# Performance work log

Measured on AMD Instinct MI355X. Metric: run time of the kernel, lower is better.

## Reference

```python
import jax, jax.numpy as jnp
import numpy as np

B = 8192
N_COLS = 64
D = 1024
EPS = 1e-5


def _layernorm(x, g, b):
    m = jnp.mean(x, axis=-1, keepdims=True)
    v = jnp.mean(jnp.square(x - m), axis=-1, keepdims=True)
    return (x - m) * jax.lax.rsqrt(v + EPS) * g + b


def setup_inputs() -> dict:
    key = jax.random.key(0)
    ks = jax.random.split(key, 8)
    s = 0.02
    return {
        "x1_enc": jax.random.normal(ks[0], (1, N_COLS, D), jnp.float32),
        "x2_enc": jax.random.normal(ks[1], (B, D), jnp.float32),
        "We": jax.random.normal(ks[2], (4, 2 * D, D), jnp.float32) * s,
        "be": jnp.zeros((4, D), jnp.float32),
        "W1": jax.random.normal(ks[3], (2 * D, 4 * D), jnp.float32) * s,
        "b1": jnp.zeros((4 * D,), jnp.float32),
        "g1": jnp.ones((4 * D,), jnp.float32),
        "bt1": jnp.zeros((4 * D,), jnp.float32),
        "W2": jax.random.normal(ks[4], (4 * D, 2 * D), jnp.float32) * s,
        "b2": jnp.zeros((2 * D,), jnp.float32),
        "g2": jnp.ones((2 * D,), jnp.float32),
        "bt2": jnp.zeros((2 * D,), jnp.float32),
        "W3": jax.random.normal(ks[5], (2 * D, 1), jnp.float32) * s,
        "b3": jnp.zeros((1,), jnp.float32),
        "col_pairs": jax.random.randint(ks[6], (B, 2), 0, N_COLS, jnp.int64),
        "vis_type": jax.random.randint(ks[7], (B,), 0, 4, jnp.int64),
    }


def reference(x1_enc, x2_enc, We, be, W1, b1, g1, bt1, W2, b2, g2, bt2, W3, b3,
              col_pairs, vis_type):
    # x1 repeated B times is identical per row -> gather directly from x1_enc[0]
    x11 = x1_enc[0, col_pairs[:, 0]]          # [B, D]
    x12 = x1_enc[0, col_pairs[:, 1]]          # [B, D]
    x1c = jnp.concatenate([x11, x12], axis=1)  # [B, 2D]

    # 1-of-4 expert routing: compute all experts, select by vis_type
    all_y = jax.nn.relu(jnp.einsum('bd,edk->bek', x1c, We) + be)  # [B, 4, D]
    y1 = jnp.take_along_axis(all_y, vis_type[:, None, None], axis=1)[:, 0]  # [B, D]

    y = jnp.concatenate([y1, x2_enc], axis=1)  # [B, 2D]
    h = _layernorm(jax.nn.relu(y @ W1 + b1), g1, bt1)
    h = _layernorm(jax.nn.relu(h @ W2 + b2), g2, bt2)
    return jax.nn.sigmoid(h @ W3 + b3)  # [B, 1]
```

## Files before the change

kernel.cpp:

```cpp
#include <hip/hip_runtime.h>

typedef unsigned short u16;
typedef __bf16 bf16x8 __attribute__((ext_vector_type(8)));
typedef float f32x4v __attribute__((ext_vector_type(4)));
typedef u16 u16x8 __attribute__((ext_vector_type(8)));

__device__ __forceinline__ u16 f2bf(float f) {
  union { float f; unsigned u; } v; v.f = f;
  unsigned r = v.u + 0x7fffu + ((v.u >> 16) & 1u);
  return (u16)(r >> 16);
}
__device__ __forceinline__ float bf2f(u16 h) {
  union { unsigned u; float f; } v; v.u = ((unsigned)h) << 16;
  return v.f;
}

#define G2L16(g, l)                                                            \
  __builtin_amdgcn_global_load_lds((__attribute__((address_space(1))) void*)(g), \
                                   (__attribute__((address_space(3))) void*)(l), 16, 0, 0)

__global__ __launch_bounds__(256) void k_transpose2(const float* __restrict__ W1,
                                                    u16* __restrict__ W1T,
                                                    const float* __restrict__ W2,
                                                    u16* __restrict__ W2gT,
                                                    const float* __restrict__ g1,
                                                    const float* __restrict__ bt1,
                                                    float* __restrict__ w2ps,
                                                    float* __restrict__ w2pc) {
  __shared__ float tile[64][65];
  int bid = blockIdx.x;
  const float* in;
  u16* out;
  int R, C, bx, by, fold;
  if (bid < 2048) {
    in = W1; out = W1T; R = 2048; C = 4096; fold = 0;
    bx = bid & 63; by = bid >> 6;
  } else {
    bid -= 2048;
    in = W2; out = W2gT; R = 4096; C = 2048; fold = 1;
    bx = bid & 31; by = bid >> 5;
  }
  const int c0 = bx * 64, r0 = by * 64;
  const int t = threadIdx.x;
  const int tc = (t & 15) * 4, tr = t >> 4;
#pragma unroll
  for (int i = 0; i < 4; ++i) {
    int r = tr + i * 16;
    f32x4v v = *(const f32x4v*)(in + (size_t)(r0 + r) * C + c0 + tc);
    tile[r][tc] = v[0]; tile[r][tc + 1] = v[1];
    tile[r][tc + 2] = v[2]; tile[r][tc + 3] = v[3];
  }
  __syncthreads();
  const int oc = t >> 2;
  const int rb = (t & 3) * 16;
  float gv[16];
#pragma unroll
  for (int i = 0; i < 16; ++i) gv[i] = fold ? g1[r0 + rb + i] : 1.f;
  u16x8 o0, o1;
#pragma unroll
  for (int i = 0; i < 8; ++i) o0[i] = f2bf(tile[rb + i][oc] * gv[i]);
#pragma unroll
  for (int i = 0; i < 8; ++i) o1[i] = f2bf(tile[rb + 8 + i][oc] * gv[8 + i]);
  *(u16x8*)(out + (size_t)(c0 + oc) * R + r0 + rb) = o0;
  *(u16x8*)(out + (size_t)(c0 + oc) * R + r0 + rb + 8) = o1;
  if (fold) {
    float ps = 0.f, pc = 0.f;
#pragma unroll
    for (int i = 0; i < 16; ++i) {
      float w = tile[rb + i][oc];
      ps += gv[i] * w;
      pc += bt1[r0 + rb + i] * w;
    }
    ps += __shfl_down(ps, 2, 4); ps += __shfl_down(ps, 1, 4);
    pc += __shfl_down(pc, 2, 4); pc += __shfl_down(pc, 1, 4);
    if ((t & 3) == 0) {
      w2ps[(size_t)by * 2048 + c0 + oc] = ps;
      w2pc[(size_t)by * 2048 + c0 + oc] = pc;
    }
  }
}

__global__ __launch_bounds__(256) void k_pq(const float* __restrict__ x1,
                                            const float* __restrict__ We,
                                            float* __restrict__ pq) {
  const int n0 = blockIdx.x * 64;
  const int ep = blockIdx.y;
  const int e = ep >> 1, p = ep & 1;
  const int chalf = blockIdx.z;
  __shared__ float As[32][33];
  __shared__ float Bs[32][68];
  const int t = threadIdx.x;
  const int tx = t & 15, ty = t >> 4;
  float acc[2][4] = {};
  const float* wbase = We + (size_t)e * 2048 * 1024 + (size_t)p * 1024 * 1024;
  for (int k0 = 0; k0 < 1024; k0 += 32) {
#pragma unroll
    for (int i = 0; i < 4; ++i) {
      int ix = t + i * 256;
      As[ix >> 5][ix & 31] =
          x1[(size_t)(chalf * 32 + (ix >> 5)) * 1024 + k0 + (ix & 31)];
    }
#pragma unroll
    for (int i = 0; i < 8; ++i) {
      int ix = t + i * 256;
      Bs[ix >> 6][ix & 63] = wbase[(size_t)(k0 + (ix >> 6)) * 1024 + n0 + (ix & 63)];
    }
    __syncthreads();
#pragma unroll
    for (int kk = 0; kk < 32; ++kk) {
      float av[2];
#pragma unroll
      for (int i = 0; i < 2; ++i) av[i] = As[ty * 2 + i][kk];
      f32x4v bv = *(const f32x4v*)&Bs[kk][tx * 4];
#pragma unroll
      for (int i = 0; i < 2; ++i)
#pragma unroll
        for (int j = 0; j < 4; ++j) acc[i][j] += av[i] * bv[j];
    }
    __syncthreads();
  }
#pragma unroll
  for (int i = 0; i < 2; ++i) {
    float* dst = pq + ((size_t)ep * 64 + chalf * 32 + ty * 2 + i) * 1024 + n0 + tx * 4;
#pragma unroll
    for (int j = 0; j < 4; ++j) dst[j] = acc[i][j];
  }
}

__global__ __launch_bounds__(256) void k_build_y(const float* __restrict__ pq,
                                                 const float* __restrict__ x2,
                                                 const float* __restrict__ be,
                                                 const int* __restrict__ cp,
                                                 const int* __restrict__ vis,
                                                 u16* __restrict__ Y) {
  const int t = threadIdx.x;
  for (int rr = 0; rr < 8; ++rr) {
    const int b = blockIdx.x * 8 + rr;
    const int e = vis[b];
    u16x8 o;
    if (t < 128) {
      const int c0 = cp[2 * b], c1 = cp[2 * b + 1];
      const size_t po = ((size_t)(e * 2) * 64 + c0) * 1024 + t * 8;
      const size_t qo = ((size_t)(e * 2 + 1) * 64 + c1) * 1024 + t * 8;
      const float* B = be + e * 1024 + t * 8;
#pragma unroll
      for (int i = 0; i < 8; ++i) {
        float v = pq[po + i] + pq[qo + i] + B[i];
        o[i] = f2bf(v > 0.f ? v : 0.f);
      }
      *(u16x8*)(Y + (size_t)b * 2048 + t * 8) = o;
    } else {
      const float* X = x2 + (size_t)b * 1024 + (size_t)(t - 128) * 8;
#pragma unroll
      for (int i = 0; i < 8; ++i) o[i] = f2bf(X[i]);
      *(u16x8*)(Y + (size_t)b * 2048 + 1024 + (size_t)(t - 128) * 8) = o;
    }
  }
}

#define BARRIER __builtin_amdgcn_s_barrier()
#define WLG0                                                    \
  do {                                                          \
    asm volatile("s_waitcnt lgkmcnt(0)" ::: "memory");          \
    __builtin_amdgcn_sched_barrier(0);                          \
  } while (0)
#define WVM(n) asm volatile("s_waitcnt vmcnt(" #n ")" ::: "memory")

template <int MODE>
__global__ __launch_bounds__(512, 2) void k_gemm(const u16* __restrict__ A,
                                                 const u16* __restrict__ BT,
                                                 const float* __restrict__ bias,
                                                 const float2* __restrict__ stats,
                                                 const float* __restrict__ s1,
                                                 const float* __restrict__ c1b,
                                                 const float* __restrict__ gw3,
                                                 float2* __restrict__ sp_out,
                                                 float4* __restrict__ part,
                                                 u16* __restrict__ C,
                                                 int M, int N, int K) {
  __shared__ u16 smem[65536];
  const int tid = threadIdx.x;
  const int lane = tid & 63;
  const int wave = tid >> 6;
  const int wm = wave >> 2;
  const int wn = wave & 3;

  const int nx = gridDim.x, ny = gridDim.y;
  const int bid = blockIdx.y * nx + blockIdx.x;
  const int stripe = ny >> 3;
  const int xcd = bid & 7;
  const int loc = bid >> 3;
  const int by = xcd * stripe + (loc % stripe);
  const int bx = loc / stripe;
  const int tileM = by * 256;
  const int tileN = bx * 256;

  f32x4v acc[8][4];
#pragma unroll
  for (int i = 0; i < 8; ++i)
#pragma unroll
    for (int j = 0; j < 4; ++j) acc[i][j] = (f32x4v){0.f, 0.f, 0.f, 0.f};

  const int srow = tid >> 3;
  const int slc = ((tid & 7) ^ (srow & 7)) * 8;
  const u16* aG = A + (size_t)(tileM + srow) * K + slc;
  const u16* bG = BT + (size_t)(tileN + srow) * K + slc;

#define STAGE(ab, h, buf, kt)                                                  \
  do {                                                                         \
    u16* dst_ = smem + (buf) * 32768 + (ab) * 16384 + (h) * 8192 + tid * 8;    \
    const u16* g_ = ((ab) ? bG : aG) + (size_t)(h) * 128 * K + (size_t)(kt) * 64; \
    G2L16(g_, dst_);                                                           \
    G2L16(g_ + (size_t)64 * K, dst_ + 4096);                                   \
  } while (0)

  const int kp0 = (((lane >> 4) ^ (lane & 7)) * 8);
  const int kp1 = kp0 ^ 32;
  const int awoff = wm * 8192 + (lane & 15) * 64;
  const int bwoff = (wn >> 1) * 8192 + ((wn & 1) * 64 + (lane & 15)) * 64;

  bf16x8 af[2][4], bfr[2][4];

#define RD_A(buf, mh)                                                          \
  do {                                                                         \
    const u16* ap_ = smem + (buf) * 32768 + awoff;                             \
    _Pragma("unroll") for (int q = 0; q < 4; ++q) {                            \
      af[0][q] = *(const bf16x8*)(ap_ + ((mh) * 4 + q) * 1024 + kp0);          \
      af[1][q] = *(const bf16x8*)(ap_ + ((mh) * 4 + q) * 1024 + kp1);          \
    }                                                                          \
  } while (0)

#define RD_B(buf, nh)                                                          \
  do {                                                                         \
    const u16* bp_ = smem + (buf) * 32768 + 16384 + bwoff;                     \
    _Pragma("unroll") for (int q = 0; q < 2; ++q) {                            \
      bfr[0][(nh) * 2 + q] = *(const bf16x8*)(bp_ + ((nh) * 2 + q) * 1024 + kp0); \
      bfr[1][(nh) * 2 + q] = *(const bf16x8*)(bp_ + ((nh) * 2 + q) * 1024 + kp1); \
    }                                                                          \
  } while (0)

#define QUAD(mh, nh)                                                           \
  do {                                                                         \
    __builtin_amdgcn_s_setprio(1);                                             \
    _Pragma("unroll") for (int kh = 0; kh < 2; ++kh)                           \
    _Pragma("unroll") for (int q = 0; q < 4; ++q)                              \
    _Pragma("unroll") for (int p = 0; p < 2; ++p)                              \
      acc[(mh) * 4 + q][(nh) * 2 + p] = __builtin_amdgcn_mfma_f32_16x16x32_bf16( \
          af[kh][q], bfr[kh][(nh) * 2 + p], acc[(mh) * 4 + q][(nh) * 2 + p], 0, 0, 0); \
    __builtin_amdgcn_s_setprio(0);                                             \
  } while (0)

  const int nkt = K >> 6;
  const int niter = nkt >> 1;

  STAGE(1, 0, 0, 0);
  STAGE(1, 1, 0, 0);
  STAGE(0, 0, 0, 0);
  STAGE(0, 1, 0, 0);
  STAGE(1, 0, 1, 1);
  STAGE(1, 1, 1, 1);
  STAGE(0, 0, 1, 1);
  WVM(6);
  BARRIER;

  for (int it = 0; it < niter; ++it) {
    const int t1 = 2 * it + 1;
    int t2 = 2 * it + 2; if (t2 >= nkt) t2 = nkt - 1;
    int t3 = 2 * it + 3; if (t3 >= nkt) t3 = nkt - 1;
    RD_A(0, 0); RD_B(0, 0);
    STAGE(0, 1, 1, t1);
    BARRIER; WLG0; QUAD(0, 0); BARRIER;
    RD_B(0, 1);
    BARRIER; WLG0; QUAD(0, 1); BARRIER;
    RD_A(0, 1);
    STAGE(1, 0, 0, t2);
    BARRIER; WLG0; QUAD(1, 0); BARRIER;
    STAGE(1, 1, 0, t2);
    STAGE(0, 0, 0, t2);
    BARRIER; QUAD(1, 1); WVM(6); BARRIER;
    RD_A(1, 0); RD_B(1, 0);
    STAGE(0, 1, 0, t2);
    BARRIER; WLG0; QUAD(0, 0); BARRIER;
    RD_B(1, 1);
    BARRIER; WLG0; QUAD(0, 1); BARRIER;
    RD_A(1, 1);
    STAGE(1, 0, 1, t3);
    BARRIER; WLG0; QUAD(1, 0); BARRIER;
    STAGE(1, 1, 1, t3);
    STAGE(0, 0, 1, t3);
    BARRIER; QUAD(1, 1); WVM(6); BARRIER;
  }

  const int crow = tileM + wm * 128 + (lane >> 4) * 4;
  const int ccol = tileN + wn * 64 + (lane & 15);
  float cv0[4], cv1[4], cg[4];
#pragma unroll
  for (int ni = 0; ni < 4; ++ni) {
    const int c = ccol + ni * 16;
    if (MODE == 0) {
      cv0[ni] = bias[c];
    } else {
      cv0[ni] = s1[c];
      cv1[ni] = c1b[c];
      cg[ni] = gw3[c];
    }
  }
  const int cb = bx * 4 + wn;
#pragma unroll
  for (int mi = 0; mi < 8; ++mi) {
#pragma unroll
    for (int r = 0; r < 4; ++r) {
      const int row = crow + mi * 16 + r;
      if (MODE == 0) {
        float s_ = 0.f, ss_ = 0.f;
#pragma unroll
        for (int ni = 0; ni < 4; ++ni) {
          float v = acc[mi][ni][r] + cv0[ni];
          v = v > 0.f ? v : 0.f;
          s_ += v; ss_ += v * v;
          C[(size_t)row * N + ccol + ni * 16] = f2bf(v);
        }
#pragma unroll
        for (int off = 8; off >= 1; off >>= 1) {
          s_ += __shfl_xor(s_, off, 16);
          ss_ += __shfl_xor(ss_, off, 16);
        }
        if ((lane & 15) == 0)
          sp_out[(size_t)row * 64 + cb] = make_float2(s_, ss_);
      } else {
        float2 st = stats[row];
        const float m = st.x, rs = st.y;
        float s_ = 0.f, ss_ = 0.f, d_ = 0.f;
#pragma unroll
        for (int ni = 0; ni < 4; ++ni) {
          float v = rs * acc[mi][ni][r] - rs * m * cv0[ni] + cv1[ni];
          v = v > 0.f ? v : 0.f;
          s_ += v; ss_ += v * v; d_ += v * cg[ni];
        }
#pragma unroll
        for (int off = 8; off >= 1; off >>= 1) {
          s_ += __shfl_xor(s_, off, 16);
          ss_ += __shfl_xor(ss_, off, 16);
          d_ += __shfl_xor(d_, off, 16);
        }
        if ((lane & 15) == 0)
          part[(size_t)row * 32 + cb] = make_float4(s_, ss_, d_, 0.f);
      }
    }
  }
}

__global__ __launch_bounds__(256) void k_reduce(const float2* __restrict__ sp,
                                                float2* __restrict__ stats,
                                                const float* __restrict__ w2ps,
                                                const float* __restrict__ w2pc,
                                                const float* __restrict__ b2,
                                                float* __restrict__ s1,
                                                float* __restrict__ c1b,
                                                const float* __restrict__ g2,
                                                const float* __restrict__ bt2,
                                                const float* __restrict__ W3,
                                                float* __restrict__ gw3,
                                                float* __restrict__ scal) {
  __shared__ float red[8];
  const int bid = blockIdx.x;
  const int t = threadIdx.x;
  if (bid < 32) {
    const int g = t >> 4, l = t & 15;
#pragma unroll 1
    for (int rr = 0; rr < 16; ++rr) {
      const int row = bid * 256 + rr * 16 + g;
      float s = 0.f, ss = 0.f;
#pragma unroll
      for (int i = 0; i < 4; ++i) {
        float2 p = sp[(size_t)row * 64 + l * 4 + i];
        s += p.x; ss += p.y;
      }
#pragma unroll
      for (int off = 8; off >= 1; off >>= 1) {
        s += __shfl_xor(s, off, 16);
        ss += __shfl_xor(ss, off, 16);
      }
      if (l == 0) {
        float m = s * (1.f / 4096.f);
        float var = ss * (1.f / 4096.f) - m * m;
        stats[row] = make_float2(m, rsqrtf(var + 1e-5f));
      }
    }
  } else if (bid < 40) {
    const int nn = (bid - 32) * 256 + t;
    float s = 0.f, c = 0.f;
    for (int kb = 0; kb < 64; ++kb) {
      s += w2ps[(size_t)kb * 2048 + nn];
      c += w2pc[(size_t)kb * 2048 + nn];
    }
    s1[nn] = s;
    c1b[nn] = c + b2[nn];
  } else {
    float sg = 0.f, cb = 0.f;
    for (int i = 0; i < 8; ++i) {
      int c = i * 256 + t;
      float w3 = W3[c];
      float gv = g2[c] * w3;
      gw3[c] = gv;
      sg += gv;
      cb += bt2[c] * w3;
    }
#pragma unroll
    for (int off = 32; off > 0; off >>= 1) {
      sg += __shfl_down(sg, off, 64);
      cb += __shfl_down(cb, off, 64);
    }
    const int lane = t & 63, wv = t >> 6;
    if (lane == 0) { red[wv] = sg; red[4 + wv] = cb; }
    __syncthreads();
    if (t == 0) {
      scal[0] = red[0] + red[1] + red[2] + red[3];
      scal[1] = red[4] + red[5] + red[6] + red[7];
    }
  }
}

__global__ __launch_bounds__(256) void k_final(const float4* __restrict__ part,
                                               const float* __restrict__ scal,
                                               const float* __restrict__ b3,
                                               float* __restrict__ out) {
  const int t = threadIdx.x;
  const int g = t >> 4, l = t & 15;
  const int row = blockIdx.x * 16 + g;
  float4 a = part[(size_t)row * 32 + l * 2];
  float4 b = part[(size_t)row * 32 + l * 2 + 1];
  float S = a.x + b.x, SS = a.y + b.y, D = a.z + b.z;
#pragma unroll
  for (int off = 8; off >= 1; off >>= 1) {
    S += __shfl_xor(S, off, 16);
    SS += __shfl_xor(SS, off, 16);
    D += __shfl_xor(D, off, 16);
  }
  if (l == 0) {
    float m = S * (1.f / 2048.f);
    float rs = rsqrtf(SS * (1.f / 2048.f) - m * m + 1e-5f);
    float logit = rs * D - rs * m * scal[0] + scal[1] + b3[0];
    out[row] = 1.f / (1.f + expf(-logit));
  }
}

extern "C" void kernel_launch(void* const* d_in, const int* in_sizes, int n_in,
                              void* d_out, int out_size, void* d_ws, size_t ws_size,
                              hipStream_t stream) {
  const float* x1 = (const float*)d_in[0];
  const float* x2 = (const float*)d_in[1];
  const float* We = (const float*)d_in[2];
  const float* be = (const float*)d_in[3];
  const float* W1 = (const float*)d_in[4];
  const float* b1 = (const float*)d_in[5];
  const float* g1 = (const float*)d_in[6];
  const float* bt1 = (const float*)d_in[7];
  const float* W2 = (const float*)d_in[8];
  const float* b2 = (const float*)d_in[9];
  const float* g2 = (const float*)d_in[10];
  const float* bt2 = (const float*)d_in[11];
  const float* W3 = (const float*)d_in[12];
  const float* b3 = (const float*)d_in[13];
  const int* cp = (const int*)d_in[14];
  const int* vis = (const int*)d_in[15];
  float* out = (float*)d_out;

  char* ws = (char*)d_ws;
  u16* W1T  = (u16*)(ws);
  u16* W2gT = (u16*)(ws + 16777216);
  u16* Y    = (u16*)(ws + 33554432);
  u16* H1   = (u16*)(ws + 67108864);
  float* PQ = (float*)(ws + 134217728);
  float2* sp = (float2*)(ws + 134217728);
  float4* part = (float4*)(ws + 134217728);
  float2* stats = (float2*)(ws + 138412032);
  float* s1   = (float*)(ws + 138477568);
  float* c1b  = (float*)(ws + 138485760);
  float* w2ps = (float*)(ws + 138493952);
  float* w2pc = (float*)(ws + 139018240);
  float* gw3  = (float*)(ws + 139542528);
  float* scal = (float*)(ws + 139550720);

  k_transpose2<<<4096, 256, 0, stream>>>(W1, W1T, W2, W2gT, g1, bt1, w2ps, w2pc);
  k_pq<<<dim3(16, 8, 2), 256, 0, stream>>>(x1, We, PQ);
  k_build_y<<<1024, 256, 0, stream>>>(PQ, x2, be, cp, vis, Y);
  k_gemm<0><<<dim3(16, 32), 512, 0, stream>>>(
      Y, W1T, b1, nullptr, nullptr, nullptr, nullptr, sp, nullptr, H1,
      8192, 4096, 2048);
  k_reduce<<<41, 256, 0, stream>>>(sp, stats, w2ps, w2pc, b2, s1, c1b,
                                   g2, bt2, W3, gw3, scal);
  k_gemm<1><<<dim3(8, 32), 512, 0, stream>>>(
      H1, W2gT, nullptr, stats, s1, c1b, gw3, nullptr, part, nullptr,
      8192, 2048, 4096);
  k_final<<<512, 256, 0, stream>>>(part, scal, b3, out);
}
```

Before: 468.9 us.

## Merge weight prep kernels and rework GEMM LDS read/stage pipeline schedule

```diff
diff --git a/kernel.cpp b/kernel.cpp
--- a/kernel.cpp
+++ b/kernel.cpp
@@ -19,111 +19,113 @@
   __builtin_amdgcn_global_load_lds((__attribute__((address_space(1))) void*)(g), \
                                    (__attribute__((address_space(3))) void*)(l), 16, 0, 0)
 
-__global__ __launch_bounds__(256) void k_transpose2(const float* __restrict__ W1,
-                                                    u16* __restrict__ W1T,
-                                                    const float* __restrict__ W2,
-                                                    u16* __restrict__ W2gT,
-                                                    const float* __restrict__ g1,
-                                                    const float* __restrict__ bt1,
-                                                    float* __restrict__ w2ps,
-                                                    float* __restrict__ w2pc) {
-  __shared__ float tile[64][65];
+__global__ __launch_bounds__(256) void k_prep(const float* __restrict__ W1,
+                                              u16* __restrict__ W1T,
+                                              const float* __restrict__ W2,
+                                              u16* __restrict__ W2gT,
+                                              const float* __restrict__ g1,
+                                              const float* __restrict__ bt1,
+                                              float* __restrict__ w2ps,
+                                              float* __restrict__ w2pc,
+                                              const float* __restrict__ x1,
+                                              const float* __restrict__ We,
+                                              float* __restrict__ pq) {
+  __shared__ float lds[4224];
   int bid = blockIdx.x;
-  const float* in;
-  u16* out;
-  int R, C, bx, by, fold;
-  if (bid < 2048) {
-    in = W1; out = W1T; R = 2048; C = 4096; fold = 0;
-    bx = bid & 63; by = bid >> 6;
+  const int t = threadIdx.x;
+  if (bid < 4096) {
+    float (*tile)[65] = (float(*)[65])lds;
+    const float* in;
+    u16* out;
+    int R, C, bx, by, fold;
+    if (bid < 2048) {
+      in = W1; out = W1T; R = 2048; C = 4096; fold = 0;
+      bx = bid & 63; by = bid >> 6;
+    } else {
+      bid -= 2048;
+      in = W2; out = W2gT; R = 4096; C = 2048; fold = 1;
+      bx = bid & 31; by = bid >> 5;
+    }
+    const int c0 = bx * 64, r0 = by * 64;
+    const int tc = (t & 15) * 4, tr = t >> 4;
+#pragma unroll
+    for (int i = 0; i < 4; ++i) {
+      int r = tr + i * 16;
+      f32x4v v = *(const f32x4v*)(in + (size_t)(r0 + r) * C + c0 + tc);
+      tile[r][tc] = v[0]; tile[r][tc + 1] = v[1];
+      tile[r][tc + 2] = v[2]; tile[r][tc + 3] = v[3];
+    }
+    __syncthreads();
+    const int oc = t >> 2;
+    const int rb = (t & 3) * 16;
+    float gv[16];
+#pragma unroll
+    for (int i = 0; i < 16; ++i) gv[i] = fold ? g1[r0 + rb + i] : 1.f;
+    u16x8 o0, o1;
+#pragma unroll
+    for (int i = 0; i < 8; ++i) o0[i] = f2bf(tile[rb + i][oc] * gv[i]);
+#pragma unroll
+    for (int i = 0; i < 8; ++i) o1[i] = f2bf(tile[rb + 8 + i][oc] * gv[8 + i]);
+    *(u16x8*)(out + (size_t)(c0 + oc) * R + r0 + rb) = o0;
+    *(u16x8*)(out + (size_t)(c0 + oc) * R + r0 + rb + 8) = o1;
+    if (fold) {
+      float ps = 0.f, pc = 0.f;
+#pragma unroll
+      for (int i = 0; i < 16; ++i) {
+        float w = tile[rb + i][oc];
+        ps += gv[i] * w;
+        pc += bt1[r0 + rb + i] * w;
+      }
+      ps += __shfl_down(ps, 2, 4); ps += __shfl_down(ps, 1, 4);
+      pc += __shfl_down(pc, 2, 4); pc += __shfl_down(pc, 1, 4);
+      if ((t & 3) == 0) {
+        w2ps[(size_t)by * 2048 + c0 + oc] = ps;
+        w2pc[(size_t)by * 2048 + c0 + oc] = pc;
+      }
+    }
   } else {
-    bid -= 2048;
-    in = W2; out = W2gT; R = 4096; C = 2048; fold = 1;
-    bx = bid & 31; by = bid >> 5;
-  }
-  const int c0 = bx * 64, r0 = by * 64;
-  const int t = threadIdx.x;
-  const int tc = (t & 15) * 4, tr = t >> 4;
-#pragma unroll
-  for (int i = 0; i < 4; ++i) {
-    int r = tr + i * 16;
-    f32x4v v = *(const f32x4v*)(in + (size_t)(r0 + r) * C + c0 + tc);
-    tile[r][tc] = v[0]; tile[r][tc + 1] = v[1];
-    tile[r][tc + 2] = v[2]; tile[r][tc + 3] = v[3];
-  }
-  __syncthreads();
-  const int oc = t >> 2;
-  const int rb = (t & 3) * 16;
-  float gv[16];
-#pragma unroll
-  for (int i = 0; i < 16; ++i) gv[i] = fold ? g1[r0 + rb + i] : 1.f;
-  u16x8 o0, o1;
-#pragma unroll
-  for (int i = 0; i < 8; ++i) o0[i] = f2bf(tile[rb + i][oc] * gv[i]);
-#pragma unroll
-  for (int i = 0; i < 8; ++i) o1[i] = f2bf(tile[rb + 8 + i][oc] * gv[8 + i]);
-  *(u16x8*)(out + (size_t)(c0 + oc) * R + r0 + rb) = o0;
-  *(u16x8*)(out + (size_t)(c0 + oc) * R + r0 + rb + 8) = o1;
-  if (fold) {
-    float ps = 0.f, pc = 0.f;
-#pragma unroll
-    for (int i = 0; i < 16; ++i) {
-      float w = tile[rb + i][oc];
-      ps += gv[i] * w;
-      pc += bt1[r0 + rb + i] * w;
-    }
-    ps += __shfl_down(ps, 2, 4); ps += __shfl_down(ps, 1, 4);
-    pc += __shfl_down(pc, 2, 4); pc += __shfl_down(pc, 1, 4);
-    if ((t & 3) == 0) {
-      w2ps[(size_t)by * 2048 + c0 + oc] = ps;
-      w2pc[(size_t)by * 2048 + c0 + oc] = pc;
-    }
-  }
-}
-
-__global__ __launch_bounds__(256) void k_pq(const float* __restrict__ x1,
-                                            const float* __restrict__ We,
-                                            float* __restrict__ pq) {
-  const int n0 = blockIdx.x * 64;
-  const int ep = blockIdx.y;
-  const int e = ep >> 1, p = ep & 1;
-  const int chalf = blockIdx.z;
-  __shared__ float As[32][33];
-  __shared__ float Bs[32][68];
-  const int t = threadIdx.x;
-  const int tx = t & 15, ty = t >> 4;
-  float acc[2][4] = {};
-  const float* wbase = We + (size_t)e * 2048 * 1024 + (size_t)p * 1024 * 1024;
-  for (int k0 = 0; k0 < 1024; k0 += 32) {
-#pragma unroll
-    for (int i = 0; i < 4; ++i) {
-      int ix = t + i * 256;
-      As[ix >> 5][ix & 31] =
-          x1[(size_t)(chalf * 32 + (ix >> 5)) * 1024 + k0 + (ix & 31)];
-    }
-#pragma unroll
-    for (int i = 0; i < 8; ++i) {
-      int ix = t + i * 256;
-      Bs[ix >> 6][ix & 63] = wbase[(size_t)(k0 + (ix >> 6)) * 1024 + n0 + (ix & 63)];
-    }
-    __syncthreads();
-#pragma unroll
-    for (int kk = 0; kk < 32; ++kk) {
-      float av[2];
-#pragma unroll
-      for (int i = 0; i < 2; ++i) av[i] = As[ty * 2 + i][kk];
-      f32x4v bv = *(const f32x4v*)&Bs[kk][tx * 4];
-#pragma unroll
-      for (int i = 0; i < 2; ++i)
-#pragma unroll
-        for (int j = 0; j < 4; ++j) acc[i][j] += av[i] * bv[j];
-    }
-    __syncthreads();
-  }
-#pragma unroll
-  for (int i = 0; i < 2; ++i) {
-    float* dst = pq + ((size_t)ep * 64 + chalf * 32 + ty * 2 + i) * 1024 + n0 + tx * 4;
-#pragma unroll
-    for (int j = 0; j < 4; ++j) dst[j] = acc[i][j];
+    const int pqb = bid - 4096;
+    const int n0 = (pqb & 15) * 64;
+    const int ep = (pqb >> 4) & 7;
+    const int e = ep >> 1, p = ep & 1;
+    const int chalf = pqb >> 7;
+    float (*As)[33] = (float(*)[33])lds;
+    float (*Bs)[68] = (float(*)[68])(lds + 32 * 33);
+    const int tx = t & 15, ty = t >> 4;
+    float acc[2][4] = {};
+    const float* wbase = We + (size_t)e * 2048 * 1024 + (size_t)p * 1024 * 1024;
+    for (int k0 = 0; k0 < 1024; k0 += 32) {
+#pragma unroll
+      for (int i = 0; i < 4; ++i) {
+        int ix = t + i * 256;
+        As[ix >> 5][ix & 31] =
+            x1[(size_t)(chalf * 32 + (ix >> 5)) * 1024 + k0 + (ix & 31)];
+      }
+#pragma unroll
+      for (int i = 0; i < 8; ++i) {
+        int ix = t + i * 256;
+        Bs[ix >> 6][ix & 63] = wbase[(size_t)(k0 + (ix >> 6)) * 1024 + n0 + (ix & 63)];
+      }
+      __syncthreads();
+#pragma unroll
+      for (int kk = 0; kk < 32; ++kk) {
+        float av[2];
+#pragma unroll
+        for (int i = 0; i < 2; ++i) av[i] = As[ty * 2 + i][kk];
+        f32x4v bv = *(const f32x4v*)&Bs[kk][tx * 4];
+#pragma unroll
+        for (int i = 0; i < 2; ++i)
+#pragma unroll
+          for (int j = 0; j < 4; ++j) acc[i][j] += av[i] * bv[j];
+      }
+      __syncthreads();
+    }
+#pragma unroll
+    for (int i = 0; i < 2; ++i) {
+      float* dst = pq + ((size_t)ep * 64 + chalf * 32 + ty * 2 + i) * 1024 + n0 + tx * 4;
+#pragma unroll
+      for (int j = 0; j < 4; ++j) dst[j] = acc[i][j];
+    }
   }
 }
 
@@ -159,11 +161,7 @@
 }
 
 #define BARRIER __builtin_amdgcn_s_barrier()
-#define WLG0                                                    \
-  do {                                                          \
-    asm volatile("s_waitcnt lgkmcnt(0)" ::: "memory");          \
-    __builtin_amdgcn_sched_barrier(0);                          \
-  } while (0)
+#define WLG(n) asm volatile("s_waitcnt lgkmcnt(" #n ")" ::: "memory")
 #define WVM(n) asm volatile("s_waitcnt vmcnt(" #n ")" ::: "memory")
 
 template <int MODE>
@@ -219,34 +217,43 @@
   const int awoff = wm * 8192 + (lane & 15) * 64;
   const int bwoff = (wn >> 1) * 8192 + ((wn & 1) * 64 + (lane & 15)) * 64;
 
-  bf16x8 af[2][4], bfr[2][4];
-
-#define RD_A(buf, mh)                                                          \
+  bf16x8 af[2][4], ag[2][4], bfr[2][4];
+
+#define RD_AF(buf)                                                             \
   do {                                                                         \
     const u16* ap_ = smem + (buf) * 32768 + awoff;                             \
     _Pragma("unroll") for (int q = 0; q < 4; ++q) {                            \
-      af[0][q] = *(const bf16x8*)(ap_ + ((mh) * 4 + q) * 1024 + kp0);          \
-      af[1][q] = *(const bf16x8*)(ap_ + ((mh) * 4 + q) * 1024 + kp1);          \
+      af[0][q] = *(const bf16x8*)(ap_ + q * 1024 + kp0);                       \
+      af[1][q] = *(const bf16x8*)(ap_ + q * 1024 + kp1);                       \
     }                                                                          \
   } while (0)
 
-#define RD_B(buf, nh)                                                          \
+#define RD_AG(buf)                                                             \
+  do {                                                                         \
+    const u16* ap_ = smem + (buf) * 32768 + awoff + 4096;                      \
+    _Pragma("unroll") for (int q = 0; q < 4; ++q) {                            \
+      ag[0][q] = *(const bf16x8*)(ap_ + q * 1024 + kp0);                       \
+      ag[1][q] = *(const bf16x8*)(ap_ + q * 1024 + kp1);                       \
+    }                                                                          \
+  } while (0)
+
+#define RD_BB(buf)                                                             \
   do {                                                                         \
     const u16* bp_ = smem + (buf) * 32768 + 16384 + bwoff;                     \
-    _Pragma("unroll") for (int q = 0; q < 2; ++q) {                            \
-      bfr[0][(nh) * 2 + q] = *(const bf16x8*)(bp_ + ((nh) * 2 + q) * 1024 + kp0); \
-      bfr[1][(nh) * 2 + q] = *(const bf16x8*)(bp_ + ((nh) * 2 + q) * 1024 + kp1); \
+    _Pragma("unroll") for (int j = 0; j < 4; ++j) {                            \
+      bfr[0][j] = *(const bf16x8*)(bp_ + j * 1024 + kp0);                      \
+      bfr[1][j] = *(const bf16x8*)(bp_ + j * 1024 + kp1);                      \
     }                                                                          \
   } while (0)
 
-#define QUAD(mh, nh)                                                           \
+#define QUAD(AF, mh, nh)                                                       \
   do {                                                                         \
     __builtin_amdgcn_s_setprio(1);                                             \
     _Pragma("unroll") for (int kh = 0; kh < 2; ++kh)                           \
     _Pragma("unroll") for (int q = 0; q < 4; ++q)                              \
     _Pragma("unroll") for (int p = 0; p < 2; ++p)                              \
       acc[(mh) * 4 + q][(nh) * 2 + p] = __builtin_amdgcn_mfma_f32_16x16x32_bf16( \
-          af[kh][q], bfr[kh][(nh) * 2 + p], acc[(mh) * 4 + q][(nh) * 2 + p], 0, 0, 0); \
+          AF[kh][q], bfr[(kh)][(nh) * 2 + p], acc[(mh) * 4 + q][(nh) * 2 + p], 0, 0, 0); \
     __builtin_amdgcn_s_setprio(0);                                             \
   } while (0)
 
@@ -259,36 +266,48 @@
   STAGE(0, 1, 0, 0);
   STAGE(1, 0, 1, 1);
   STAGE(1, 1, 1, 1);
-  STAGE(0, 0, 1, 1);
-  WVM(6);
-  BARRIER;
+  WVM(4);
 
   for (int it = 0; it < niter; ++it) {
     const int t1 = 2 * it + 1;
     int t2 = 2 * it + 2; if (t2 >= nkt) t2 = nkt - 1;
     int t3 = 2 * it + 3; if (t3 >= nkt) t3 = nkt - 1;
-    RD_A(0, 0); RD_B(0, 0);
+    BARRIER;
+    RD_AF(0); RD_BB(0);
+    STAGE(0, 0, 1, t1);
+    WLG(4);
+    QUAD(af, 0, 0);
+    BARRIER;
+    RD_AG(0);
     STAGE(0, 1, 1, t1);
-    BARRIER; WLG0; QUAD(0, 0); BARRIER;
-    RD_B(0, 1);
-    BARRIER; WLG0; QUAD(0, 1); BARRIER;
-    RD_A(0, 1);
+    WLG(8);
+    QUAD(af, 0, 1);
+    BARRIER;
     STAGE(1, 0, 0, t2);
-    BARRIER; WLG0; QUAD(1, 0); BARRIER;
+    WLG(0);
+    QUAD(ag, 1, 0);
+    BARRIER;
     STAGE(1, 1, 0, t2);
+    QUAD(ag, 1, 1);
+    WVM(4);
+    BARRIER;
+    RD_AF(1); RD_BB(1);
     STAGE(0, 0, 0, t2);
-    BARRIER; QUAD(1, 1); WVM(6); BARRIER;
-    RD_A(1, 0); RD_B(1, 0);
+    WLG(4);
+    QUAD(af, 0, 0);
+    BARRIER;
+    RD_AG(1);
     STAGE(0, 1, 0, t2);
-    BARRIER; WLG0; QUAD(0, 0); BARRIER;
-    RD_B(1, 1);
-    BARRIER; WLG0; QUAD(0, 1); BARRIER;
-    RD_A(1, 1);
+    WLG(8);
+    QUAD(af, 0, 1);
+    BARRIER;
     STAGE(1, 0, 1, t3);
-    BARRIER; WLG0; QUAD(1, 0); BARRIER;
+    WLG(0);
+    QUAD(ag, 1, 0);
+    BARRIER;
     STAGE(1, 1, 1, t3);
-    STAGE(0, 0, 1, t3);
-    BARRIER; QUAD(1, 1); WVM(6); BARRIER;
+    QUAD(ag, 1, 1);
+    WVM(4);
   }
 
   const int crow = tileM + wm * 128 + (lane >> 4) * 4;
@@ -482,8 +501,8 @@
   float* gw3  = (float*)(ws + 139542528);
   float* scal = (float*)(ws + 139550720);
 
-  k_transpose2<<<4096, 256, 0, stream>>>(W1, W1T, W2, W2gT, g1, bt1, w2ps, w2pc);
-  k_pq<<<dim3(16, 8, 2), 256, 0, stream>>>(x1, We, PQ);
+  k_prep<<<4352, 256, 0, stream>>>(W1, W1T, W2, W2gT, g1, bt1, w2ps, w2pc,
+                                   x1, We, PQ);
   k_build_y<<<1024, 256, 0, stream>>>(PQ, x2, be, cp, vis, Y);
   k_gemm<0><<<dim3(16, 32), 512, 0, stream>>>(
       Y, W1T, b1, nullptr, nullptr, nullptr, nullptr, sp, nullptr, H1,
```

Result: faster. 454.2 us (-3.2%).
